# Optimization experiments

Hardware: AMD Instinct MI355X
Metric: run time of the kernel (lower is better)

Reference implementation:

```python
import jax, jax.numpy as jnp
import numpy as np
from jax import lax

N_VOX = 100000   # occupied voxels
GRID = 160       # dense grid extent per axis
K = 5            # kernel size -> 125 offsets
K3 = K * K * K
IMG_C, PTS_C, OUT_C = 64, 32, 16
EPS = 1e-5


def _build_coords_and_kernel_map():
    """Random unique voxel coords + kernel map: nbr[n,k] = row index of voxel at
    coords[n]+offset[k], or N_VOX (sentinel -> zero feature) if unoccupied."""
    rng = np.random.default_rng(0)
    flat = rng.choice(GRID ** 3, size=N_VOX, replace=False)
    coords = np.stack(np.unravel_index(flat, (GRID, GRID, GRID)), axis=1).astype(np.int64)
    B = GRID + 4  # shift coords by +2 so offsets in [-2,2] never wrap
    enc = ((coords[:, 0] + 2) * B + (coords[:, 1] + 2)) * B + (coords[:, 2] + 2)
    order = np.argsort(enc)
    enc_s = enc[order]
    offs = np.stack(np.meshgrid(np.arange(-2, 3), np.arange(-2, 3), np.arange(-2, 3), indexing='ij'), axis=-1).reshape(-1, 3)
    nbr = np.full((N_VOX, K3), N_VOX, dtype=np.int32)
    for k, (dx, dy, dz) in enumerate(offs):
        qe = enc + ((dx * B + dy) * B + dz)
        pos = np.clip(np.searchsorted(enc_s, qe), 0, N_VOX - 1)
        hit = enc_s[pos] == qe
        nbr[:, k] = np.where(hit, order[pos].astype(np.int32), np.int32(N_VOX))
    return nbr


def setup_inputs() -> dict:
    nbr_idx = jnp.asarray(_build_coords_and_kernel_map())
    key = jax.random.key(0)
    ks = jax.random.split(key, 20)
    def w(k, shape, fan):
        return jax.random.normal(k, shape, jnp.float32) * (1.0 / np.sqrt(fan))
    def bn(k0, k1, k2, k3):
        g = jax.random.uniform(k0, (OUT_C,), jnp.float32) + 0.5
        b = jax.random.normal(k1, (OUT_C,), jnp.float32) * 0.1
        m = jax.random.normal(k2, (OUT_C,), jnp.float32) * 0.1
        v = jax.random.uniform(k3, (OUT_C,), jnp.float32) + 0.5
        return g, b, m, v
    bn_img = bn(ks[2], ks[3], ks[4], ks[5])
    bn_pts = bn(ks[7], ks[8], ks[9], ks[10])
    bn_vis = bn(ks[12], ks[13], ks[14], ks[15])
    return {
        'img_voxel_feats': jax.random.normal(ks[0], (N_VOX, IMG_C), jnp.float32),
        'pts_voxel_feats': jax.random.normal(ks[1], (N_VOX, PTS_C), jnp.float32),
        'nbr_idx': nbr_idx,
        'W_img': w(ks[16], (K3, IMG_C, OUT_C), K3 * IMG_C),
        'bn_img_g': bn_img[0], 'bn_img_b': bn_img[1], 'bn_img_m': bn_img[2], 'bn_img_v': bn_img[3],
        'W_pts': w(ks[17], (K3, PTS_C, OUT_C), K3 * PTS_C),
        'bn_pts_g': bn_pts[0], 'bn_pts_b': bn_pts[1], 'bn_pts_m': bn_pts[2], 'bn_pts_v': bn_pts[3],
        'W_vis1': w(ks[18], (K3, 2 * OUT_C, OUT_C), K3 * 2 * OUT_C),
        'bn_vis_g': bn_vis[0], 'bn_vis_b': bn_vis[1], 'bn_vis_m': bn_vis[2], 'bn_vis_v': bn_vis[3],
        'W_vis2': w(ks[19], (OUT_C, 1), OUT_C),
    }


def _sparse_conv(feats, W, nbr_idx):
    # gather-GEMM-scatter sparse conv; sentinel row N -> zero feature
    feats_pad = jnp.concatenate([feats, jnp.zeros((1, feats.shape[1]), feats.dtype)], axis=0)
    init = jnp.zeros((feats.shape[0], W.shape[2]), feats.dtype)
    def step(acc, wk_ik):
        W_k, idx_k = wk_ik  # [Cin,Cout], [N]
        return acc + feats_pad[idx_k] @ W_k, None
    out, _ = lax.scan(step, init, (W, nbr_idx.T))
    return out


def _bn_relu(x, g, b, m, v):
    return jax.nn.relu((x - m) * (g * lax.rsqrt(v + EPS)) + b)


def reference(img_voxel_feats, pts_voxel_feats, nbr_idx,
              W_img, bn_img_g, bn_img_b, bn_img_m, bn_img_v,
              W_pts, bn_pts_g, bn_pts_b, bn_pts_m, bn_pts_v,
              W_vis1, bn_vis_g, bn_vis_b, bn_vis_m, bn_vis_v,
              W_vis2):
    img = _bn_relu(_sparse_conv(img_voxel_feats, W_img, nbr_idx), bn_img_g, bn_img_b, bn_img_m, bn_img_v)
    pts = _bn_relu(_sparse_conv(pts_voxel_feats, W_pts, nbr_idx), bn_pts_g, bn_pts_b, bn_pts_m, bn_pts_v)
    cat = jnp.concatenate([img, pts], axis=1)  # [N, 2*OUT_C]
    h = _bn_relu(_sparse_conv(cat, W_vis1, nbr_idx), bn_vis_g, bn_vis_b, bn_vis_m, bn_vis_v)
    vis_w = jax.nn.sigmoid(h @ W_vis2)  # [N,1]
    return vis_w * img + (1.0 - vis_w) * pts
```

## Files before the change

### kernel.cpp

```cpp
#include <hip/hip_runtime.h>

#define N_VOX 100000
#define K3 125
#define IMG_C 64
#define PTS_C 32
#define OUT_C 16
#define EPSF 1e-5f

#define WIT 0
#define WPT 128000
#define WVT 192000
#define CATOFF 256000

__global__ __launch_bounds__(256) void prep_transpose(
    const float* __restrict__ Wi, const float* __restrict__ Wp,
    const float* __restrict__ Wv, float* __restrict__ ws)
{
    int i = blockIdx.x * 256 + threadIdx.x;
    if (i < 125 * 64 * 16) {
        int k = i >> 10, r = i & 1023;
        int c = r >> 4, o = r & 15;
        int cs = c >> 4, t = (c >> 2) & 3, e = c & 3;
        ws[WIT + k * 1024 + t * 256 + (cs * 16 + o) * 4 + e] = Wi[i];
    }
    if (i < 125 * 32 * 16) {
        int k = i / 512, r = i % 512;
        int c = r >> 4, o = r & 15;
        int cs = c >> 3, t = (c >> 2) & 1, e = c & 3;
        ws[WPT + k * 512 + t * 256 + (cs * 16 + o) * 4 + e] = Wp[i];
        ws[WVT + k * 512 + t * 256 + (cs * 16 + o) * 4 + e] = Wv[i];
    }
}

__global__ __launch_bounds__(256) void convA(
    const float* __restrict__ fimg, const float* __restrict__ fpts,
    const int* __restrict__ nbr, float* __restrict__ ws,
    const float* __restrict__ gi, const float* __restrict__ bi,
    const float* __restrict__ mi, const float* __restrict__ vi,
    const float* __restrict__ gp, const float* __restrict__ bp,
    const float* __restrict__ mp, const float* __restrict__ vp)
{
    int wid = threadIdx.x >> 6;
    int lane = threadIdx.x & 63;
    int n = blockIdx.x * 4 + wid;
    if (n >= N_VOX) return;
    int o = lane & 15, cs = lane >> 4;

    __shared__ float lds[4][96];
    float* fs = lds[wid];

    const float* __restrict__ Wi = ws + WIT;
    const float* __restrict__ Wp = ws + WPT;
    float* __restrict__ cat = ws + CATOFF;

    float accI = 0.f, accP = 0.f;

    const int* row = nbr + (long)n * K3;
    #pragma unroll
    for (int h = 0; h < 2; ++h) {
        int kl = h * 64 + lane;
        int idx = (kl < K3) ? row[kl] : N_VOX;
        unsigned long long mask = __ballot(idx < N_VOX);
        while (mask) {
            int b = __builtin_ctzll(mask);
            mask &= mask - 1;
            int j = __shfl(idx, b);
            int k = h * 64 + b;
            fs[lane] = fimg[(long)j * IMG_C + lane];
            if (lane < 32) fs[64 + lane] = fpts[(long)j * PTS_C + lane];
            const float4* wi4 = (const float4*)(Wi + k * 1024);
            const float4* f4  = (const float4*)(fs + cs * 16);
            #pragma unroll
            for (int t = 0; t < 4; ++t) {
                float4 w = wi4[t * 64 + lane], f = f4[t];
                accI += w.x * f.x + w.y * f.y + w.z * f.z + w.w * f.w;
            }
            const float4* wp4 = (const float4*)(Wp + k * 512);
            const float4* fp4 = (const float4*)(fs + 64 + cs * 8);
            #pragma unroll
            for (int t = 0; t < 2; ++t) {
                float4 w = wp4[t * 64 + lane], f = fp4[t];
                accP += w.x * f.x + w.y * f.y + w.z * f.z + w.w * f.w;
            }
        }
    }
    accI += __shfl_xor(accI, 16); accI += __shfl_xor(accI, 32);
    accP += __shfl_xor(accP, 16); accP += __shfl_xor(accP, 32);

    if (lane < 16) {
        float si = gi[o] * rsqrtf(vi[o] + EPSF);
        float xi = fmaxf((accI - mi[o]) * si + bi[o], 0.f);
        float sp = gp[o] * rsqrtf(vp[o] + EPSF);
        float xp = fmaxf((accP - mp[o]) * sp + bp[o], 0.f);
        cat[(long)n * 32 + o] = xi;
        cat[(long)n * 32 + 16 + o] = xp;
    }
}

__global__ __launch_bounds__(256) void convB(
    const int* __restrict__ nbr, const float* __restrict__ ws,
    const float* __restrict__ gv, const float* __restrict__ bv,
    const float* __restrict__ mv, const float* __restrict__ vv,
    const float* __restrict__ w2, float* __restrict__ out)
{
    int wid = threadIdx.x >> 6;
    int lane = threadIdx.x & 63;
    int n = blockIdx.x * 4 + wid;
    if (n >= N_VOX) return;
    int o = lane & 15, cs = lane >> 4;

    __shared__ float lds[4][32];
    float* fs = lds[wid];

    const float* __restrict__ Wv = ws + WVT;
    const float* __restrict__ cat = ws + CATOFF;

    float acc = 0.f;
    const int* row = nbr + (long)n * K3;
    #pragma unroll
    for (int h = 0; h < 2; ++h) {
        int kl = h * 64 + lane;
        int idx = (kl < K3) ? row[kl] : N_VOX;
        unsigned long long mask = __ballot(idx < N_VOX);
        while (mask) {
            int b = __builtin_ctzll(mask);
            mask &= mask - 1;
            int j = __shfl(idx, b);
            int k = h * 64 + b;
            if (lane < 32) fs[lane] = cat[(long)j * 32 + lane];
            const float4* wv4 = (const float4*)(Wv + k * 512);
            const float4* f4  = (const float4*)(fs + cs * 8);
            #pragma unroll
            for (int t = 0; t < 2; ++t) {
                float4 w = wv4[t * 64 + lane], f = f4[t];
                acc += w.x * f.x + w.y * f.y + w.z * f.z + w.w * f.w;
            }
        }
    }
    acc += __shfl_xor(acc, 16); acc += __shfl_xor(acc, 32);

    float s = gv[o] * rsqrtf(vv[o] + EPSF);
    float hh = fmaxf((acc - mv[o]) * s + bv[o], 0.f);
    float p = hh * w2[o];
    p += __shfl_xor(p, 1); p += __shfl_xor(p, 2);
    p += __shfl_xor(p, 4); p += __shfl_xor(p, 8);
    float vis = 1.f / (1.f + __expf(-p));

    if (lane < 16) {
        float xi = cat[(long)n * 32 + o];
        float xp = cat[(long)n * 32 + 16 + o];
        out[(long)n * 16 + o] = vis * xi + (1.f - vis) * xp;
    }
}

extern "C" void kernel_launch(void* const* d_in, const int* in_sizes, int n_in,
                              void* d_out, int out_size, void* d_ws, size_t ws_size,
                              hipStream_t stream) {
    const float* fimg = (const float*)d_in[0];
    const float* fpts = (const float*)d_in[1];
    const int*   nbr  = (const int*)d_in[2];
    const float* Wimg = (const float*)d_in[3];
    const float* gi = (const float*)d_in[4];
    const float* bi = (const float*)d_in[5];
    const float* mi = (const float*)d_in[6];
    const float* vi = (const float*)d_in[7];
    const float* Wpts = (const float*)d_in[8];
    const float* gp = (const float*)d_in[9];
    const float* bp = (const float*)d_in[10];
    const float* mp = (const float*)d_in[11];
    const float* vp = (const float*)d_in[12];
    const float* Wvis = (const float*)d_in[13];
    const float* gv = (const float*)d_in[14];
    const float* bv = (const float*)d_in[15];
    const float* mv = (const float*)d_in[16];
    const float* vv = (const float*)d_in[17];
    const float* w2 = (const float*)d_in[18];
    float* out = (float*)d_out;
    float* ws = (float*)d_ws;

    hipLaunchKernelGGL(prep_transpose, dim3(500), dim3(256), 0, stream,
                       Wimg, Wpts, Wvis, ws);
    hipLaunchKernelGGL(convA, dim3(N_VOX / 4), dim3(256), 0, stream,
                       fimg, fpts, nbr, ws, gi, bi, mi, vi, gp, bp, mp, vp);
    hipLaunchKernelGGL(convB, dim3(N_VOX / 4), dim3(256), 0, stream,
                       nbr, ws, gv, bv, mv, vv, w2, out);
}
```

Before: 202.5 us.

## Replace per-voxel neighbor gather with per-offset pair lists and atomic scatter

The kernel map is now compacted into per-offset lists of (output, input) pairs, using an atomic counter per offset. Scatter kernels then keep each offset's weights in LDS, multiply the gathered neighbor features and atomically add the results into accumulators. The center offset is handled densely in separate finalize kernels that also apply BN, ReLU and the fusion gate. This targets the cost of each wave scanning all 125 mostly empty map entries with serialized loops. In exchange it adds atomic contention on counters and accumulators, more kernel launches, and a fixed per-offset capacity of 4096 that silently drops pairs on denser inputs.

New measurement: 263.6 us. 1.3x slower.

```diff
diff --git a/kernel.cpp b/kernel.cpp
--- a/kernel.cpp
+++ b/kernel.cpp
@@ -2,154 +2,235 @@
 
 #define N_VOX 100000
 #define K3 125
-#define IMG_C 64
-#define PTS_C 32
-#define OUT_C 16
+#define CENTER_K 62
+#define CAP 4096
 #define EPSF 1e-5f
 
 #define WIT 0
 #define WPT 128000
 #define WVT 192000
-#define CATOFF 256000
-
-__global__ __launch_bounds__(256) void prep_transpose(
+#define CNT 256000
+#define PRS 258048
+#define ACC 1282048
+#define ACV 4482048
+#define CAT 6082048
+
+#define DOT4(a, w) ((a).x*(w).x + (a).y*(w).y + (a).z*(w).z + (a).w*(w).w)
+
+__global__ __launch_bounds__(256) void prep(
     const float* __restrict__ Wi, const float* __restrict__ Wp,
     const float* __restrict__ Wv, float* __restrict__ ws)
 {
-    int i = blockIdx.x * 256 + threadIdx.x;
-    if (i < 125 * 64 * 16) {
-        int k = i >> 10, r = i & 1023;
-        int c = r >> 4, o = r & 15;
-        int cs = c >> 4, t = (c >> 2) & 3, e = c & 3;
-        ws[WIT + k * 1024 + t * 256 + (cs * 16 + o) * 4 + e] = Wi[i];
-    }
-    if (i < 125 * 32 * 16) {
-        int k = i / 512, r = i % 512;
-        int c = r >> 4, o = r & 15;
-        int cs = c >> 3, t = (c >> 2) & 1, e = c & 3;
-        ws[WPT + k * 512 + t * 256 + (cs * 16 + o) * 4 + e] = Wp[i];
-        ws[WVT + k * 512 + t * 256 + (cs * 16 + o) * 4 + e] = Wv[i];
-    }
-}
-
-__global__ __launch_bounds__(256) void convA(
+    const int NZ = 2048 + 3200000 + 1600000;
+    for (int i = blockIdx.x * 256 + threadIdx.x; i < NZ; i += gridDim.x * 256) {
+        int a = (i < 2048) ? (CNT + i) : (ACC + i - 2048);
+        ws[a] = 0.f;
+        if (i < 128000) {
+            int k = i >> 10, r = i & 1023;
+            int c = r >> 4, o = r & 15;
+            int cs = c >> 4, t = (c >> 2) & 3, e = c & 3;
+            ws[WIT + k * 1024 + t * 256 + (cs * 16 + o) * 4 + e] = Wi[i];
+        }
+        if (i < 64000) {
+            int k = i / 512, r = i % 512;
+            int c = r >> 4, o = r & 15;
+            int cs = c >> 3, t = (c >> 2) & 1, e = c & 3;
+            ws[WPT + k * 512 + t * 256 + (cs * 16 + o) * 4 + e] = Wp[i];
+            ws[WVT + k * 512 + t * 256 + (cs * 16 + o) * 4 + e] = Wv[i];
+        }
+    }
+}
+
+__global__ __launch_bounds__(256) void build_pairs(const int* __restrict__ nbr,
+                                                   float* __restrict__ ws)
+{
+    int* cnt = (int*)(ws + CNT);
+    int2* pairs = (int2*)(ws + PRS);
+    const int TOT = N_VOX * K3;
+    for (int i = blockIdx.x * 256 + threadIdx.x; i < TOT; i += gridDim.x * 256) {
+        int idx = nbr[i];
+        int k = i % K3;
+        if (idx < N_VOX && k != CENTER_K) {
+            int n = i / K3;
+            int pos = atomicAdd(&cnt[k * 16], 1);
+            if (pos < CAP) pairs[k * CAP + pos] = make_int2(n, idx);
+        }
+    }
+}
+
+__global__ __launch_bounds__(256) void scatterA(
     const float* __restrict__ fimg, const float* __restrict__ fpts,
-    const int* __restrict__ nbr, float* __restrict__ ws,
+    float* __restrict__ ws)
+{
+    int k = blockIdx.x;
+    __shared__ float Wl[1536];
+    {
+        int tid = threadIdx.x;
+        #pragma unroll
+        for (int t = 0; t < 4; ++t) Wl[t * 256 + tid] = ws[WIT + k * 1024 + t * 256 + tid];
+        #pragma unroll
+        for (int t = 0; t < 2; ++t) Wl[1024 + t * 256 + tid] = ws[WPT + k * 512 + t * 256 + tid];
+    }
+    __syncthreads();
+    int cnt = ((const int*)(ws + CNT))[k * 16];
+    if (cnt > CAP) cnt = CAP;
+    int chunk = (cnt + gridDim.y - 1) / gridDim.y;
+    int start = blockIdx.y * chunk;
+    int end = min(start + chunk, cnt);
+    int wid = threadIdx.x >> 6, lane = threadIdx.x & 63;
+    int cs = lane >> 4;
+    const int2* __restrict__ pairs = (const int2*)(ws + PRS) + k * CAP;
+    const float4* __restrict__ fi4 = (const float4*)fimg;
+    const float4* __restrict__ fp4 = (const float4*)fpts;
+    const float4* W4 = (const float4*)Wl;
+    float* __restrict__ acc = ws + ACC;
+
+    int p = start + wid;
+    float4 A0, A1, A2, A3, P0, P1;
+    int n = 0;
+    if (p < end) {
+        int2 pr = pairs[p]; n = pr.x;
+        const float4* r = fi4 + pr.y * 16 + cs * 4;
+        A0 = r[0]; A1 = r[1]; A2 = r[2]; A3 = r[3];
+        const float4* q = fp4 + pr.y * 8 + cs * 2;
+        P0 = q[0]; P1 = q[1];
+    }
+    while (p < end) {
+        int pn = p + 4;
+        int2 prn = make_int2(0, 0);
+        if (pn < end) prn = pairs[pn];
+        float4 w;
+        float aI, aP;
+        w = W4[lane];            aI  = DOT4(A0, w);
+        w = W4[64 + lane];       aI += DOT4(A1, w);
+        w = W4[128 + lane];      aI += DOT4(A2, w);
+        w = W4[192 + lane];      aI += DOT4(A3, w);
+        w = W4[256 + lane];      aP  = DOT4(P0, w);
+        w = W4[320 + lane];      aP += DOT4(P1, w);
+        int ncur = n;
+        if (pn < end) {
+            n = prn.x;
+            const float4* r = fi4 + prn.y * 16 + cs * 4;
+            A0 = r[0]; A1 = r[1]; A2 = r[2]; A3 = r[3];
+            const float4* q = fp4 + prn.y * 8 + cs * 2;
+            P0 = q[0]; P1 = q[1];
+        }
+        aI += __shfl_xor(aI, 16); aI += __shfl_xor(aI, 32);
+        aP += __shfl_xor(aP, 16); aP += __shfl_xor(aP, 32);
+        if (lane < 32) atomicAdd(&acc[ncur * 32 + lane], lane < 16 ? aI : aP);
+        p = pn;
+    }
+}
+
+__global__ __launch_bounds__(256) void finalizeA(
+    const float* __restrict__ fimg, const float* __restrict__ fpts,
+    float* __restrict__ ws,
     const float* __restrict__ gi, const float* __restrict__ bi,
     const float* __restrict__ mi, const float* __restrict__ vi,
     const float* __restrict__ gp, const float* __restrict__ bp,
     const float* __restrict__ mp, const float* __restrict__ vp)
 {
-    int wid = threadIdx.x >> 6;
-    int lane = threadIdx.x & 63;
+    int wid = threadIdx.x >> 6, lane = threadIdx.x & 63;
     int n = blockIdx.x * 4 + wid;
     if (n >= N_VOX) return;
     int o = lane & 15, cs = lane >> 4;
-
-    __shared__ float lds[4][96];
-    float* fs = lds[wid];
-
-    const float* __restrict__ Wi = ws + WIT;
-    const float* __restrict__ Wp = ws + WPT;
-    float* __restrict__ cat = ws + CATOFF;
-
-    float accI = 0.f, accP = 0.f;
-
-    const int* row = nbr + (long)n * K3;
+    const float4* fi4 = (const float4*)fimg + n * 16 + cs * 4;
+    const float4* fp4 = (const float4*)fpts + n * 8 + cs * 2;
+    const float4* wi4 = (const float4*)(ws + WIT + CENTER_K * 1024);
+    const float4* wp4 = (const float4*)(ws + WPT + CENTER_K * 512);
+    float aI = 0.f, aP = 0.f;
     #pragma unroll
-    for (int h = 0; h < 2; ++h) {
-        int kl = h * 64 + lane;
-        int idx = (kl < K3) ? row[kl] : N_VOX;
-        unsigned long long mask = __ballot(idx < N_VOX);
-        while (mask) {
-            int b = __builtin_ctzll(mask);
-            mask &= mask - 1;
-            int j = __shfl(idx, b);
-            int k = h * 64 + b;
-            fs[lane] = fimg[(long)j * IMG_C + lane];
-            if (lane < 32) fs[64 + lane] = fpts[(long)j * PTS_C + lane];
-            const float4* wi4 = (const float4*)(Wi + k * 1024);
-            const float4* f4  = (const float4*)(fs + cs * 16);
-            #pragma unroll
-            for (int t = 0; t < 4; ++t) {
-                float4 w = wi4[t * 64 + lane], f = f4[t];
-                accI += w.x * f.x + w.y * f.y + w.z * f.z + w.w * f.w;
-            }
-            const float4* wp4 = (const float4*)(Wp + k * 512);
-            const float4* fp4 = (const float4*)(fs + 64 + cs * 8);
-            #pragma unroll
-            for (int t = 0; t < 2; ++t) {
-                float4 w = wp4[t * 64 + lane], f = fp4[t];
-                accP += w.x * f.x + w.y * f.y + w.z * f.z + w.w * f.w;
-            }
-        }
-    }
-    accI += __shfl_xor(accI, 16); accI += __shfl_xor(accI, 32);
-    accP += __shfl_xor(accP, 16); accP += __shfl_xor(accP, 32);
-
-    if (lane < 16) {
-        float si = gi[o] * rsqrtf(vi[o] + EPSF);
-        float xi = fmaxf((accI - mi[o]) * si + bi[o], 0.f);
-        float sp = gp[o] * rsqrtf(vp[o] + EPSF);
-        float xp = fmaxf((accP - mp[o]) * sp + bp[o], 0.f);
-        cat[(long)n * 32 + o] = xi;
-        cat[(long)n * 32 + 16 + o] = xp;
-    }
-}
-
-__global__ __launch_bounds__(256) void convB(
-    const int* __restrict__ nbr, const float* __restrict__ ws,
+    for (int t = 0; t < 4; ++t) { float4 f = fi4[t], w = wi4[t * 64 + lane]; aI += DOT4(f, w); }
+    #pragma unroll
+    for (int t = 0; t < 2; ++t) { float4 f = fp4[t], w = wp4[t * 64 + lane]; aP += DOT4(f, w); }
+    aI += __shfl_xor(aI, 16); aI += __shfl_xor(aI, 32);
+    aP += __shfl_xor(aP, 16); aP += __shfl_xor(aP, 32);
+    if (lane < 32) {
+        float tot = ws[ACC + n * 32 + lane] + (lane < 16 ? aI : aP);
+        float g, b, m, v;
+        if (lane < 16) { g = gi[o]; b = bi[o]; m = mi[o]; v = vi[o]; }
+        else           { g = gp[o]; b = bp[o]; m = mp[o]; v = vp[o]; }
+        float y = fmaxf((tot - m) * (g * rsqrtf(v + EPSF)) + b, 0.f);
+        ws[CAT + n * 32 + lane] = y;
+    }
+}
+
+__global__ __launch_bounds__(256) void scatterV(float* __restrict__ ws)
+{
+    int k = blockIdx.x;
+    __shared__ float Wl[512];
+    {
+        int tid = threadIdx.x;
+        #pragma unroll
+        for (int t = 0; t < 2; ++t) Wl[t * 256 + tid] = ws[WVT + k * 512 + t * 256 + tid];
+    }
+    __syncthreads();
+    int cnt = ((const int*)(ws + CNT))[k * 16];
+    if (cnt > CAP) cnt = CAP;
+    int chunk = (cnt + gridDim.y - 1) / gridDim.y;
+    int start = blockIdx.y * chunk;
+    int end = min(start + chunk, cnt);
+    int wid = threadIdx.x >> 6, lane = threadIdx.x & 63;
+    int cs = lane >> 4;
+    const int2* __restrict__ pairs = (const int2*)(ws + PRS) + k * CAP;
+    const float4* __restrict__ c4 = (const float4*)(ws + CAT);
+    const float4* W4 = (const float4*)Wl;
+    float* __restrict__ accV = ws + ACV;
+
+    int p = start + wid;
+    float4 C0, C1;
+    int n = 0;
+    if (p < end) {
+        int2 pr = pairs[p]; n = pr.x;
+        const float4* r = c4 + pr.y * 8 + cs * 2;
+        C0 = r[0]; C1 = r[1];
+    }
+    while (p < end) {
+        int pn = p + 4;
+        int2 prn = make_int2(0, 0);
+        if (pn < end) prn = pairs[pn];
+        float4 w;
+        float aV;
+        w = W4[lane];       aV  = DOT4(C0, w);
+        w = W4[64 + lane];  aV += DOT4(C1, w);
+        int ncur = n;
+        if (pn < end) {
+            n = prn.x;
+            const float4* r = c4 + prn.y * 8 + cs * 2;
+            C0 = r[0]; C1 = r[1];
+        }
+        aV += __shfl_xor(aV, 16); aV += __shfl_xor(aV, 32);
+        if (lane < 16) atomicAdd(&accV[ncur * 16 + lane], aV);
+        p = pn;
+    }
+}
+
+__global__ __launch_bounds__(256) void finalizeB(
+    float* __restrict__ ws,
     const float* __restrict__ gv, const float* __restrict__ bv,
     const float* __restrict__ mv, const float* __restrict__ vv,
     const float* __restrict__ w2, float* __restrict__ out)
 {
-    int wid = threadIdx.x >> 6;
-    int lane = threadIdx.x & 63;
+    int wid = threadIdx.x >> 6, lane = threadIdx.x & 63;
     int n = blockIdx.x * 4 + wid;
     if (n >= N_VOX) return;
     int o = lane & 15, cs = lane >> 4;
-
-    __shared__ float lds[4][32];
-    float* fs = lds[wid];
-
-    const float* __restrict__ Wv = ws + WVT;
-    const float* __restrict__ cat = ws + CATOFF;
-
-    float acc = 0.f;
-    const int* row = nbr + (long)n * K3;
+    const float4* c4 = (const float4*)(ws + CAT) + n * 8 + cs * 2;
+    const float4* wv4 = (const float4*)(ws + WVT + CENTER_K * 512);
+    float aV = 0.f;
     #pragma unroll
-    for (int h = 0; h < 2; ++h) {
-        int kl = h * 64 + lane;
-        int idx = (kl < K3) ? row[kl] : N_VOX;
-        unsigned long long mask = __ballot(idx < N_VOX);
-        while (mask) {
-            int b = __builtin_ctzll(mask);
-            mask &= mask - 1;
-            int j = __shfl(idx, b);
-            int k = h * 64 + b;
-            if (lane < 32) fs[lane] = cat[(long)j * 32 + lane];
-            const float4* wv4 = (const float4*)(Wv + k * 512);
-            const float4* f4  = (const float4*)(fs + cs * 8);
-            #pragma unroll
-            for (int t = 0; t < 2; ++t) {
-                float4 w = wv4[t * 64 + lane], f = f4[t];
-                acc += w.x * f.x + w.y * f.y + w.z * f.z + w.w * f.w;
-            }
-        }
-    }
-    acc += __shfl_xor(acc, 16); acc += __shfl_xor(acc, 32);
-
-    float s = gv[o] * rsqrtf(vv[o] + EPSF);
-    float hh = fmaxf((acc - mv[o]) * s + bv[o], 0.f);
-    float p = hh * w2[o];
-    p += __shfl_xor(p, 1); p += __shfl_xor(p, 2);
-    p += __shfl_xor(p, 4); p += __shfl_xor(p, 8);
-    float vis = 1.f / (1.f + __expf(-p));
-
+    for (int t = 0; t < 2; ++t) { float4 f = c4[t], w = wv4[t * 64 + lane]; aV += DOT4(f, w); }
+    aV += __shfl_xor(aV, 16); aV += __shfl_xor(aV, 32);
+    float sv = ws[ACV + n * 16 + o] + aV;
+    float h = fmaxf((sv - mv[o]) * (gv[o] * rsqrtf(vv[o] + EPSF)) + bv[o], 0.f);
+    float ph = h * w2[o];
+    ph += __shfl_xor(ph, 1); ph += __shfl_xor(ph, 2);
+    ph += __shfl_xor(ph, 4); ph += __shfl_xor(ph, 8);
+    float vis = 1.f / (1.f + expf(-ph));
     if (lane < 16) {
-        float xi = cat[(long)n * 32 + o];
-        float xp = cat[(long)n * 32 + 16 + o];
-        out[(long)n * 16 + o] = vis * xi + (1.f - vis) * xp;
+        float xi = ws[CAT + n * 32 + o];
+        float xp = ws[CAT + n * 32 + 16 + o];
+        out[n * 16 + o] = vis * xi + (1.f - vis) * xp;
     }
 }
 
@@ -178,10 +259,12 @@
     float* out = (float*)d_out;
     float* ws = (float*)d_ws;
 
-    hipLaunchKernelGGL(prep_transpose, dim3(500), dim3(256), 0, stream,
-                       Wimg, Wpts, Wvis, ws);
-    hipLaunchKernelGGL(convA, dim3(N_VOX / 4), dim3(256), 0, stream,
-                       fimg, fpts, nbr, ws, gi, bi, mi, vi, gp, bp, mp, vp);
-    hipLaunchKernelGGL(convB, dim3(N_VOX / 4), dim3(256), 0, stream,
-                       nbr, ws, gv, bv, mv, vv, w2, out);
-}
+    hipLaunchKernelGGL(prep, dim3(2346), dim3(256), 0, stream, Wimg, Wpts, Wvis, ws);
+    hipLaunchKernelGGL(build_pairs, dim3(6104), dim3(256), 0, stream, nbr, ws);
+    hipLaunchKernelGGL(scatterA, dim3(125, 16), dim3(256), 0, stream, fimg, fpts, ws);
+    hipLaunchKernelGGL(finalizeA, dim3(25000), dim3(256), 0, stream,
+                       fimg, fpts, ws, gi, bi, mi, vi, gp, bp, mp, vp);
+    hipLaunchKernelGGL(scatterV, dim3(125, 16), dim3(256), 0, stream, ws);
+    hipLaunchKernelGGL(finalizeB, dim3(25000), dim3(256), 0, stream,
+                       ws, gv, bv, mv, vv, w2, out);
+}
```

## Bucket neighbor pairs by kernel offset per voxel block for weight-stationary conv

Applied to the files above, without the earlier changes.

Replaces the per-voxel, per-warp gather loop with a block-level scheme. Each block of 128 voxels builds a compacted list of (voxel, neighbor) pairs grouped by kernel offset using LDS atomics and a prefix scan. Warps then claim offsets dynamically, keep that offset's weights in registers, and accumulate into LDS with atomics. The center offset is handled densely, and the list is saved to the workspace so the second conv reuses it instead of rescanning nbr_idx. This is meant to cut repeated weight reloads and wasted work on sentinel neighbors. It adds LDS atomic contention, several block-wide syncs, and a fixed 768-entry list buffer that assumes sparse occupancy.

New measurement: 229.7 us. 1.13x slower.

```diff
diff --git a/kernel.cpp b/kernel.cpp
--- a/kernel.cpp
+++ b/kernel.cpp
@@ -2,15 +2,18 @@
 
 #define N_VOX 100000
 #define K3 125
-#define IMG_C 64
-#define PTS_C 32
-#define OUT_C 16
+#define CENTER_K 62
+#define BVOX 128
+#define NBLK 782
 #define EPSF 1e-5f
 
 #define WIT 0
 #define WPT 128000
 #define WVT 192000
-#define CATOFF 256000
+#define LST 256000
+#define CAT (256000 + NBLK * 1024)
+
+#define DOT4(f_, g_) ((f_).x*(g_).x + (f_).y*(g_).y + (f_).z*(g_).z + (f_).w*(g_).w)
 
 __global__ __launch_bounds__(256) void prep_transpose(
     const float* __restrict__ Wi, const float* __restrict__ Wp,
@@ -32,7 +35,7 @@
     }
 }
 
-__global__ __launch_bounds__(256) void convA(
+__global__ __launch_bounds__(512, 6) void convA(
     const float* __restrict__ fimg, const float* __restrict__ fpts,
     const int* __restrict__ nbr, float* __restrict__ ws,
     const float* __restrict__ gi, const float* __restrict__ bi,
@@ -40,116 +43,222 @@
     const float* __restrict__ gp, const float* __restrict__ bp,
     const float* __restrict__ mp, const float* __restrict__ vp)
 {
-    int wid = threadIdx.x >> 6;
-    int lane = threadIdx.x & 63;
-    int n = blockIdx.x * 4 + wid;
-    if (n >= N_VOX) return;
-    int o = lane & 15, cs = lane >> 4;
-
-    __shared__ float lds[4][96];
-    float* fs = lds[wid];
-
-    const float* __restrict__ Wi = ws + WIT;
-    const float* __restrict__ Wp = ws + WPT;
-    float* __restrict__ cat = ws + CATOFF;
-
-    float accI = 0.f, accP = 0.f;
-
-    const int* row = nbr + (long)n * K3;
-    #pragma unroll
-    for (int h = 0; h < 2; ++h) {
-        int kl = h * 64 + lane;
-        int idx = (kl < K3) ? row[kl] : N_VOX;
-        unsigned long long mask = __ballot(idx < N_VOX);
-        while (mask) {
-            int b = __builtin_ctzll(mask);
-            mask &= mask - 1;
-            int j = __shfl(idx, b);
-            int k = h * 64 + b;
-            fs[lane] = fimg[(long)j * IMG_C + lane];
-            if (lane < 32) fs[64 + lane] = fpts[(long)j * PTS_C + lane];
-            const float4* wi4 = (const float4*)(Wi + k * 1024);
-            const float4* f4  = (const float4*)(fs + cs * 16);
-            #pragma unroll
-            for (int t = 0; t < 4; ++t) {
-                float4 w = wi4[t * 64 + lane], f = f4[t];
-                accI += w.x * f.x + w.y * f.y + w.z * f.z + w.w * f.w;
-            }
-            const float4* wp4 = (const float4*)(Wp + k * 512);
-            const float4* fp4 = (const float4*)(fs + 64 + cs * 8);
-            #pragma unroll
-            for (int t = 0; t < 2; ++t) {
-                float4 w = wp4[t * 64 + lane], f = fp4[t];
-                accP += w.x * f.x + w.y * f.y + w.z * f.z + w.w * f.w;
-            }
-        }
-    }
-    accI += __shfl_xor(accI, 16); accI += __shfl_xor(accI, 32);
-    accP += __shfl_xor(accP, 16); accP += __shfl_xor(accP, 32);
-
-    if (lane < 16) {
-        float si = gi[o] * rsqrtf(vi[o] + EPSF);
-        float xi = fmaxf((accI - mi[o]) * si + bi[o], 0.f);
-        float sp = gp[o] * rsqrtf(vp[o] + EPSF);
-        float xp = fmaxf((accP - mp[o]) * sp + bp[o], 0.f);
-        cat[(long)n * 32 + o] = xi;
-        cat[(long)n * 32 + 16 + o] = xp;
-    }
-}
-
-__global__ __launch_bounds__(256) void convB(
-    const int* __restrict__ nbr, const float* __restrict__ ws,
+    __shared__ int s_kcnt[128];
+    __shared__ int s_scan[128];
+    __shared__ int s_koff[128];
+    __shared__ int s_list[768];
+    __shared__ float s_acc[BVOX][32];
+    __shared__ int s_next;
+
+    const int tid = threadIdx.x, lane = tid & 63, wv = tid >> 6;
+    const int blk = blockIdx.x;
+    const int gbase = blk * BVOX;
+    const int vcount = min(BVOX, N_VOX - gbase);
+    const int q = lane >> 4;
+
+    if (tid < 128) s_kcnt[tid] = 0;
+    if (tid == 0) s_next = 0;
+    __syncthreads();
+
+    const int TOTE = vcount * K3;
+    const int* nrow = nbr + (size_t)gbase * K3;
+    for (int e = tid; e < TOTE; e += 512) {
+        int idx = nrow[e];
+        int k = e % K3;
+        if (idx < N_VOX && k != CENTER_K) atomicAdd(&s_kcnt[k], 1);
+    }
+    __syncthreads();
+
+    if (tid < 128) s_scan[tid] = (tid < K3) ? s_kcnt[tid] : 0;
+    __syncthreads();
+    for (int d = 1; d < 128; d <<= 1) {
+        int v = 0;
+        if (tid < 128 && tid >= d) v = s_scan[tid - d];
+        __syncthreads();
+        if (tid < 128) s_scan[tid] += v;
+        __syncthreads();
+    }
+    if (tid < 128) s_koff[tid] = (tid == 0) ? 0 : s_scan[tid - 1];
+    __syncthreads();
+    if (tid < 128) s_kcnt[tid] = s_koff[tid];
+    __syncthreads();
+
+    for (int e = tid; e < TOTE; e += 512) {
+        int idx = nrow[e];
+        int k = e % K3;
+        if (idx < N_VOX && k != CENTER_K) {
+            int ln = e / K3;
+            int pos = atomicAdd(&s_kcnt[k], 1);
+            s_list[pos] = (ln << 17) | idx;
+        }
+    }
+    __syncthreads();
+
+    {
+        int tot = s_koff[K3];
+        int* dst = (int*)(ws + LST) + (size_t)blk * 1024;
+        if (tid < 126) dst[tid] = s_koff[tid];
+        for (int p = tid; p < tot; p += 512) dst[128 + p] = s_list[p];
+    }
+
+    const float4* __restrict__ fi4 = (const float4*)fimg;
+    const float4* __restrict__ fp4 = (const float4*)fpts;
+
+    {
+        float4 cwi[4], cwp[2];
+        const float4* WI4 = (const float4*)(ws + WIT + CENTER_K * 1024);
+        const float4* WP4 = (const float4*)(ws + WPT + CENTER_K * 512);
+        #pragma unroll
+        for (int t = 0; t < 4; ++t) cwi[t] = WI4[t * 64 + lane];
+        #pragma unroll
+        for (int t = 0; t < 2; ++t) cwp[t] = WP4[t * 64 + lane];
+        for (int i = 0; i < 16; ++i) {
+            int ln = wv * 16 + i;
+            if (ln >= vcount) break;
+            int n = gbase + ln;
+            const float4* fr = fi4 + (size_t)n * 16 + q * 4;
+            const float4* gr = fp4 + (size_t)n * 8 + q * 2;
+            float aI = DOT4(fr[0], cwi[0]) + DOT4(fr[1], cwi[1])
+                     + DOT4(fr[2], cwi[2]) + DOT4(fr[3], cwi[3]);
+            float aP = DOT4(gr[0], cwp[0]) + DOT4(gr[1], cwp[1]);
+            aI += __shfl_xor(aI, 16); aI += __shfl_xor(aI, 32);
+            aP += __shfl_xor(aP, 16); aP += __shfl_xor(aP, 32);
+            if (lane < 32) s_acc[ln][lane] = (lane < 16) ? aI : aP;
+        }
+    }
+    __syncthreads();
+
+    while (true) {
+        int s;
+        if (lane == 0) s = atomicAdd(&s_next, 1);
+        s = __shfl(s, 0);
+        if (s >= K3) break;
+        int pbeg = s_koff[s], pend = s_koff[s + 1];
+        if (pbeg == pend) continue;
+        float4 swi[4], swp[2];
+        const float4* WI4 = (const float4*)(ws + WIT + s * 1024);
+        const float4* WP4 = (const float4*)(ws + WPT + s * 512);
+        #pragma unroll
+        for (int t = 0; t < 4; ++t) swi[t] = WI4[t * 64 + lane];
+        #pragma unroll
+        for (int t = 0; t < 2; ++t) swp[t] = WP4[t * 64 + lane];
+        for (int p = pbeg; p < pend; ++p) {
+            int ent = s_list[p];
+            int ln = ent >> 17, j = ent & 0x1FFFF;
+            const float4* fr = fi4 + (size_t)j * 16 + q * 4;
+            const float4* gr = fp4 + (size_t)j * 8 + q * 2;
+            float aI = DOT4(fr[0], swi[0]) + DOT4(fr[1], swi[1])
+                     + DOT4(fr[2], swi[2]) + DOT4(fr[3], swi[3]);
+            float aP = DOT4(gr[0], swp[0]) + DOT4(gr[1], swp[1]);
+            aI += __shfl_xor(aI, 16); aI += __shfl_xor(aI, 32);
+            aP += __shfl_xor(aP, 16); aP += __shfl_xor(aP, 32);
+            if (lane < 32) atomicAdd(&s_acc[ln][lane], (lane < 16) ? aI : aP);
+        }
+    }
+    __syncthreads();
+
+    {
+        int c = tid & 31;
+        float g, b, m, v;
+        if (c < 16) { g = gi[c]; b = bi[c]; m = mi[c]; v = vi[c]; }
+        else        { g = gp[c - 16]; b = bp[c - 16]; m = mp[c - 16]; v = vp[c - 16]; }
+        float sc = g * rsqrtf(v + EPSF);
+        float* cat = ws + CAT;
+        for (int r = 0; r < 8; ++r) {
+            int ln = (tid >> 5) + r * 16;
+            if (ln < vcount)
+                cat[(size_t)(gbase + ln) * 32 + c] =
+                    fmaxf((s_acc[ln][c] - m) * sc + b, 0.f);
+        }
+    }
+}
+
+__global__ __launch_bounds__(512, 6) void convB(
+    float* __restrict__ ws,
     const float* __restrict__ gv, const float* __restrict__ bv,
     const float* __restrict__ mv, const float* __restrict__ vv,
     const float* __restrict__ w2, float* __restrict__ out)
 {
-    int wid = threadIdx.x >> 6;
-    int lane = threadIdx.x & 63;
-    int n = blockIdx.x * 4 + wid;
-    if (n >= N_VOX) return;
-    int o = lane & 15, cs = lane >> 4;
-
-    __shared__ float lds[4][32];
-    float* fs = lds[wid];
-
-    const float* __restrict__ Wv = ws + WVT;
-    const float* __restrict__ cat = ws + CATOFF;
-
-    float acc = 0.f;
-    const int* row = nbr + (long)n * K3;
-    #pragma unroll
-    for (int h = 0; h < 2; ++h) {
-        int kl = h * 64 + lane;
-        int idx = (kl < K3) ? row[kl] : N_VOX;
-        unsigned long long mask = __ballot(idx < N_VOX);
-        while (mask) {
-            int b = __builtin_ctzll(mask);
-            mask &= mask - 1;
-            int j = __shfl(idx, b);
-            int k = h * 64 + b;
-            if (lane < 32) fs[lane] = cat[(long)j * 32 + lane];
-            const float4* wv4 = (const float4*)(Wv + k * 512);
-            const float4* f4  = (const float4*)(fs + cs * 8);
-            #pragma unroll
-            for (int t = 0; t < 2; ++t) {
-                float4 w = wv4[t * 64 + lane], f = f4[t];
-                acc += w.x * f.x + w.y * f.y + w.z * f.z + w.w * f.w;
+    __shared__ int s_koff[128];
+    __shared__ int s_list[768];
+    __shared__ float s_acc[BVOX][16];
+    __shared__ int s_next;
+
+    const int tid = threadIdx.x, lane = tid & 63, wv = tid >> 6;
+    const int blk = blockIdx.x;
+    const int gbase = blk * BVOX;
+    const int vcount = min(BVOX, N_VOX - gbase);
+    const int q = lane >> 4, o = lane & 15;
+
+    const int* src = (const int*)(ws + LST) + (size_t)blk * 1024;
+    if (tid < 126) s_koff[tid] = src[tid];
+    if (tid == 0) s_next = 0;
+    __syncthreads();
+    int tot = s_koff[K3];
+    for (int p = tid; p < tot; p += 512) s_list[p] = src[128 + p];
+
+    const float4* __restrict__ c4 = (const float4*)(ws + CAT);
+
+    {
+        float4 cwv[2];
+        const float4* WV4 = (const float4*)(ws + WVT + CENTER_K * 512);
+        #pragma unroll
+        for (int t = 0; t < 2; ++t) cwv[t] = WV4[t * 64 + lane];
+        for (int i = 0; i < 16; ++i) {
+            int ln = wv * 16 + i;
+            if (ln >= vcount) break;
+            int n = gbase + ln;
+            const float4* cr = c4 + (size_t)n * 8 + q * 2;
+            float aV = DOT4(cr[0], cwv[0]) + DOT4(cr[1], cwv[1]);
+            aV += __shfl_xor(aV, 16); aV += __shfl_xor(aV, 32);
+            if (lane < 16) s_acc[ln][o] = aV;
+        }
+    }
+    __syncthreads();
+
+    while (true) {
+        int s;
+        if (lane == 0) s = atomicAdd(&s_next, 1);
+        s = __shfl(s, 0);
+        if (s >= K3) break;
+        int pbeg = s_koff[s], pend = s_koff[s + 1];
+        if (pbeg == pend) continue;
+        float4 swv[2];
+        const float4* WV4 = (const float4*)(ws + WVT + s * 512);
+        #pragma unroll
+        for (int t = 0; t < 2; ++t) swv[t] = WV4[t * 64 + lane];
+        for (int p = pbeg; p < pend; ++p) {
+            int ent = s_list[p];
+            int ln = ent >> 17, j = ent & 0x1FFFF;
+            const float4* cr = c4 + (size_t)j * 8 + q * 2;
+            float aV = DOT4(cr[0], swv[0]) + DOT4(cr[1], swv[1]);
+            aV += __shfl_xor(aV, 16); aV += __shfl_xor(aV, 32);
+            if (lane < 16) atomicAdd(&s_acc[ln][o], aV);
+        }
+    }
+    __syncthreads();
+
+    {
+        float sV = gv[o] * rsqrtf(vv[o] + EPSF);
+        float bV = bv[o], mV = mv[o], w2_ = w2[o];
+        const float* cat = ws + CAT;
+        for (int r = 0; r < 4; ++r) {
+            int ln = (tid >> 4) + r * 32;
+            float h = 0.f, xi = 0.f, xp = 0.f;
+            if (ln < vcount) {
+                int n = gbase + ln;
+                h = fmaxf((s_acc[ln][o] - mV) * sV + bV, 0.f);
+                xi = cat[(size_t)n * 32 + o];
+                xp = cat[(size_t)n * 32 + 16 + o];
             }
-        }
-    }
-    acc += __shfl_xor(acc, 16); acc += __shfl_xor(acc, 32);
-
-    float s = gv[o] * rsqrtf(vv[o] + EPSF);
-    float hh = fmaxf((acc - mv[o]) * s + bv[o], 0.f);
-    float p = hh * w2[o];
-    p += __shfl_xor(p, 1); p += __shfl_xor(p, 2);
-    p += __shfl_xor(p, 4); p += __shfl_xor(p, 8);
-    float vis = 1.f / (1.f + __expf(-p));
-
-    if (lane < 16) {
-        float xi = cat[(long)n * 32 + o];
-        float xp = cat[(long)n * 32 + 16 + o];
-        out[(long)n * 16 + o] = vis * xi + (1.f - vis) * xp;
+            float ph = h * w2_;
+            ph += __shfl_xor(ph, 1); ph += __shfl_xor(ph, 2);
+            ph += __shfl_xor(ph, 4); ph += __shfl_xor(ph, 8);
+            if (ln < vcount) {
+                float vis = 1.f / (1.f + expf(-ph));
+                out[(size_t)(gbase + ln) * 16 + o] = vis * xi + (1.f - vis) * xp;
+            }
+        }
     }
 }
 
@@ -180,8 +289,8 @@
 
     hipLaunchKernelGGL(prep_transpose, dim3(500), dim3(256), 0, stream,
                        Wimg, Wpts, Wvis, ws);
-    hipLaunchKernelGGL(convA, dim3(N_VOX / 4), dim3(256), 0, stream,
+    hipLaunchKernelGGL(convA, dim3(NBLK), dim3(512), 0, stream,
                        fimg, fpts, nbr, ws, gi, bi, mi, vi, gp, bp, mp, vp);
-    hipLaunchKernelGGL(convB, dim3(N_VOX / 4), dim3(256), 0, stream,
-                       nbr, ws, gv, bv, mv, vv, w2, out);
-}
+    hipLaunchKernelGGL(convB, dim3(NBLK), dim3(512), 0, stream,
+                       ws, gv, bv, mv, vv, w2, out);
+}
```
